# Performance work log

Measured on AMD Instinct MI355X. Metric: run time of the kernel, lower is better.

The kernel has to match this reference:

```python
import jax, jax.numpy as jnp
import numpy as np

N = 500_000          # total nodes in the batched graph
B = 4096             # number of graphs
D_NODE = 256         # node_feature_size
D_GRAPH = 256        # graph_feature_size
D_LOGIT = 10         # logit_mlp_sizes[0]


def setup_inputs() -> dict:
    key = jax.random.key(0)
    ks = jax.random.split(key, 12)
    s = 0.05
    node_feats = jax.random.normal(ks[0], (N, D_NODE), dtype=jnp.float32)
    graph_feats = jax.random.normal(ks[1], (B, D_GRAPH), dtype=jnp.float32)
    segment_ids = jnp.sort(jax.random.randint(ks[2], (N,), 0, B)).astype(jnp.int64)
    # message MLP: Linear(node -> graph)
    W_msg = jax.random.normal(ks[3], (D_GRAPH, D_NODE), dtype=jnp.float32) * s
    b_msg = jnp.zeros((D_GRAPH,), dtype=jnp.float32)
    # logit MLP: Linear(node+graph -> 10) -> LeakyReLU -> Linear(10 -> 1) -> LeakyReLU
    W_l1 = jax.random.normal(ks[4], (D_LOGIT, D_NODE + D_GRAPH), dtype=jnp.float32) * s
    b_l1 = jnp.zeros((D_LOGIT,), dtype=jnp.float32)
    W_l2 = jax.random.normal(ks[5], (1, D_LOGIT), dtype=jnp.float32) * s
    b_l2 = jnp.zeros((1,), dtype=jnp.float32)
    # GRUCell(graph, graph): torch layout [3H, H] gates ordered (r, z, n)
    W_ih = jax.random.normal(ks[6], (3 * D_GRAPH, D_GRAPH), dtype=jnp.float32) * s
    W_hh = jax.random.normal(ks[7], (3 * D_GRAPH, D_GRAPH), dtype=jnp.float32) * s
    b_ih = jnp.zeros((3 * D_GRAPH,), dtype=jnp.float32)
    b_hh = jnp.zeros((3 * D_GRAPH,), dtype=jnp.float32)
    return dict(node_feats=node_feats, graph_feats=graph_feats, segment_ids=segment_ids,
                W_msg=W_msg, b_msg=b_msg, W_l1=W_l1, b_l1=b_l1, W_l2=W_l2, b_l2=b_l2,
                W_ih=W_ih, W_hh=W_hh, b_ih=b_ih, b_hh=b_hh)


def _segment_softmax(logits, seg, num_segments):
    # logits: [N, 1]; stable softmax per graph
    m = jax.ops.segment_max(logits, seg, num_segments=num_segments)      # [B,1]
    m = jnp.where(jnp.isfinite(m), m, 0.0)                               # empty segments
    ex = jnp.exp(logits - m[seg])                                        # [N,1]
    denom = jax.ops.segment_sum(ex, seg, num_segments=num_segments)      # [B,1]
    return ex / jnp.maximum(denom[seg], 1e-30)


def reference(node_feats, graph_feats, segment_ids, W_msg, b_msg,
              W_l1, b_l1, W_l2, b_l2, W_ih, W_hh, b_ih, b_hh):
    seg = segment_ids.astype(jnp.int32)
    num_graphs = graph_feats.shape[0]

    # (1) node logits: MLP on [broadcast(relu(graph_feats)), node_feats]
    g_bcast = jax.nn.relu(graph_feats)[seg]                              # [N, Dg]
    x = jnp.concatenate([g_bcast, node_feats], axis=1)                   # [N, Dg+Dn]
    h = jax.nn.leaky_relu(x @ W_l1.T + b_l1)                             # [N, 10]
    logits = jax.nn.leaky_relu(h @ W_l2.T + b_l2)                        # [N, 1]

    # (2) per-graph softmax over nodes
    alpha = _segment_softmax(logits, seg, num_graphs)                    # [N, 1]

    # (3) messages
    m = node_feats @ W_msg.T + b_msg                                     # [N, Dg]

    # (4) context: weighted segment sum
    context = jax.ops.segment_sum(alpha * m, seg, num_segments=num_graphs)  # [B, Dg]

    # (5) GRU update (torch GRUCell, gate order r,z,n)
    H = graph_feats.shape[1]
    gi = context @ W_ih.T + b_ih                                         # [B, 3H]
    gh = graph_feats @ W_hh.T + b_hh                                     # [B, 3H]
    i_r, i_z, i_n = gi[:, :H], gi[:, H:2*H], gi[:, 2*H:]
    h_r, h_z, h_n = gh[:, :H], gh[:, H:2*H], gh[:, 2*H:]
    r = jax.nn.sigmoid(i_r + h_r)
    z = jax.nn.sigmoid(i_z + h_z)
    n = jnp.tanh(i_n + r * h_n)
    return (1.0 - z) * n + z * graph_feats
```

## Files before the change

### kernel.cpp

```cpp
#include <hip/hip_runtime.h>
#include <math.h>

#define DG 256
#define DL 10
#define CHUNK 128

__device__ __forceinline__ float leaky(float x) { return x > 0.f ? x : 0.01f * x; }
__device__ __forceinline__ float sigmoidf(float x) { return 1.f / (1.f + expf(-x)); }

__global__ void k_starts(const int* __restrict__ seg, int* __restrict__ starts, int N, int B) {
  const int stride = (seg[N - 1] == 0) ? 2 : 1;
  int b = blockIdx.x * blockDim.x + threadIdx.x;
  if (b > B) return;
  if (b == B) { starts[B] = N; return; }
  int lo = 0, hi = N;
  while (lo < hi) {
    int mid = (lo + hi) >> 1;
    if (seg[(size_t)mid * stride] < b) lo = mid + 1; else hi = mid;
  }
  starts[b] = lo;
}

__global__ void k_glog(const float* __restrict__ gf, const float* __restrict__ W_l1,
                       const float* __restrict__ b_l1, float* __restrict__ glog) {
  int b = blockIdx.x;
  int l = threadIdx.x;
  float4 g4 = *(const float4*)(gf + (size_t)b * DG + 4 * l);
  g4.x = fmaxf(g4.x, 0.f); g4.y = fmaxf(g4.y, 0.f);
  g4.z = fmaxf(g4.z, 0.f); g4.w = fmaxf(g4.w, 0.f);
  float p[DL];
#pragma unroll
  for (int j = 0; j < DL; ++j) {
    float4 w4 = *(const float4*)(W_l1 + (size_t)j * 512 + 4 * l);
    p[j] = g4.x * w4.x + g4.y * w4.y + g4.z * w4.z + g4.w * w4.w;
  }
#pragma unroll
  for (int m = 32; m >= 1; m >>= 1) {
#pragma unroll
    for (int j = 0; j < DL; ++j) p[j] += __shfl_xor(p[j], m);
  }
  if (l == 0) {
#pragma unroll
    for (int j = 0; j < DL; ++j) glog[b * DL + j] = p[j] + b_l1[j];
  }
}

__global__ void k_transpose(const float* __restrict__ in, float* __restrict__ out, int R, int C) {
  int idx = blockIdx.x * blockDim.x + threadIdx.x;
  if (idx >= R * C) return;
  int r = idx / C, c = idx - r * C;
  out[c * R + r] = in[idx];
}

__global__ __launch_bounds__(256) void k_pool(
    const float* __restrict__ nf, const int* __restrict__ starts,
    const float* __restrict__ glog, const float* __restrict__ W_l1,
    const float* __restrict__ W_l2, const float* __restrict__ b_l2_p,
    float* __restrict__ pooled) {
  __shared__ float slog[CHUNK];
  __shared__ float sex[CHUNK];

  const int b = blockIdx.x;
  const int tid = threadIdx.x;
  const int lane = tid & 63;
  const int wave = tid >> 6;

  const int start = starts[b];
  const int end   = starts[b + 1];

  float wl[DL][4];
#pragma unroll
  for (int j = 0; j < DL; ++j) {
    float4 w4 = *(const float4*)(W_l1 + (size_t)j * 512 + 256 + 4 * lane);
    wl[j][0] = w4.x; wl[j][1] = w4.y; wl[j][2] = w4.z; wl[j][3] = w4.w;
  }
  float gl[DL];
#pragma unroll
  for (int j = 0; j < DL; ++j) gl[j] = glog[b * DL + j];
  float wl2[DL];
#pragma unroll
  for (int j = 0; j < DL; ++j) wl2[j] = W_l2[j];
  const float bl2 = b_l2_p[0];

  float M = -INFINITY;
  float denom = 0.f;
  float pool = 0.f;

  for (int c0 = start; c0 < end; c0 += CHUNK) {
    const int cn = min(CHUNK, end - c0);

    for (int n = wave; n < cn; n += 4) {
      const float4 x4 = *(const float4*)(nf + ((size_t)(c0 + n) << 8) + 4 * lane);
      float p[DL];
#pragma unroll
      for (int j = 0; j < DL; ++j)
        p[j] = x4.x * wl[j][0] + x4.y * wl[j][1] + x4.z * wl[j][2] + x4.w * wl[j][3];
#pragma unroll
      for (int m = 32; m >= 1; m >>= 1) {
#pragma unroll
        for (int j = 0; j < DL; ++j) p[j] += __shfl_xor(p[j], m);
      }
      float lg = bl2;
#pragma unroll
      for (int j = 0; j < DL; ++j) {
        float h = leaky(p[j] + gl[j]);
        lg += h * wl2[j];
      }
      lg = leaky(lg);
      if (lane == 0) slog[n] = lg;
    }
    __syncthreads();

    float mc = -INFINITY;
    for (int n = 0; n < cn; ++n) mc = fmaxf(mc, slog[n]);
    const float Mn = fmaxf(M, mc);
    const float sc = expf(M - Mn);
    pool *= sc;
    denom *= sc;
    M = Mn;
    if (tid < cn) sex[tid] = expf(slog[tid] - Mn);
    __syncthreads();

    float dsum = 0.f;
    for (int n = 0; n < cn; ++n) dsum += sex[n];
    denom += dsum;

    const float* rowp = nf + ((size_t)c0 << 8) + tid;
#pragma unroll 4
    for (int n = 0; n < cn; ++n) {
      pool += sex[n] * rowp[(size_t)n << 8];
    }
    __syncthreads();
  }

  pooled[(size_t)b * 256 + tid] = pool / fmaxf(denom, 1e-30f);
}

__global__ __launch_bounds__(256) void k_gru(
    const float* __restrict__ pooled, const float* __restrict__ gf,
    const float* __restrict__ WmsgT, const float* __restrict__ b_msg,
    const float* __restrict__ WihT, const float* __restrict__ WhhT,
    const float* __restrict__ b_ih, const float* __restrict__ b_hh,
    float* __restrict__ out) {
  __shared__ float pool_s[8][256];
  __shared__ float gf_s[8][256];
  __shared__ float ctx_s[8][256];

  const int t = threadIdx.x;
  const int b0 = blockIdx.x * 8;
  const int dt = t & 63;
  const int g0 = (t >> 6) * 2;

#pragma unroll
  for (int g = 0; g < 8; ++g) {
    pool_s[g][t] = pooled[(size_t)(b0 + g) * 256 + t];
    gf_s[g][t]   = gf[(size_t)(b0 + g) * 256 + t];
  }
  __syncthreads();

  {
    float acc[2][4] = {{0.f,0.f,0.f,0.f},{0.f,0.f,0.f,0.f}};
#pragma unroll 4
    for (int k = 0; k < 256; ++k) {
      float4 w = *(const float4*)(WmsgT + (size_t)k * 256 + 4 * dt);
#pragma unroll
      for (int gi = 0; gi < 2; ++gi) {
        float p = pool_s[g0 + gi][k];
        acc[gi][0] += p * w.x; acc[gi][1] += p * w.y;
        acc[gi][2] += p * w.z; acc[gi][3] += p * w.w;
      }
    }
    float4 bm = *(const float4*)(b_msg + 4 * dt);
#pragma unroll
    for (int gi = 0; gi < 2; ++gi) {
      ctx_s[g0 + gi][4 * dt + 0] = acc[gi][0] + bm.x;
      ctx_s[g0 + gi][4 * dt + 1] = acc[gi][1] + bm.y;
      ctx_s[g0 + gi][4 * dt + 2] = acc[gi][2] + bm.z;
      ctx_s[g0 + gi][4 * dt + 3] = acc[gi][3] + bm.w;
    }
  }
  __syncthreads();

  float r[2][4], z[2][4];

#pragma unroll
  for (int s = 0; s < 2; ++s) {
    float ai[2][4] = {{0.f,0.f,0.f,0.f},{0.f,0.f,0.f,0.f}};
    float ah[2][4] = {{0.f,0.f,0.f,0.f},{0.f,0.f,0.f,0.f}};
#pragma unroll 4
    for (int k = 0; k < 256; ++k) {
      float4 wi = *(const float4*)(WihT + (size_t)k * 768 + s * 256 + 4 * dt);
      float4 wh = *(const float4*)(WhhT + (size_t)k * 768 + s * 256 + 4 * dt);
#pragma unroll
      for (int gi = 0; gi < 2; ++gi) {
        float c = ctx_s[g0 + gi][k];
        float h = gf_s[g0 + gi][k];
        ai[gi][0] += c * wi.x; ai[gi][1] += c * wi.y; ai[gi][2] += c * wi.z; ai[gi][3] += c * wi.w;
        ah[gi][0] += h * wh.x; ah[gi][1] += h * wh.y; ah[gi][2] += h * wh.z; ah[gi][3] += h * wh.w;
      }
    }
    float4 bi = *(const float4*)(b_ih + s * 256 + 4 * dt);
    float4 bh = *(const float4*)(b_hh + s * 256 + 4 * dt);
#pragma unroll
    for (int gi = 0; gi < 2; ++gi) {
      float v0 = sigmoidf(ai[gi][0] + bi.x + ah[gi][0] + bh.x);
      float v1 = sigmoidf(ai[gi][1] + bi.y + ah[gi][1] + bh.y);
      float v2 = sigmoidf(ai[gi][2] + bi.z + ah[gi][2] + bh.z);
      float v3 = sigmoidf(ai[gi][3] + bi.w + ah[gi][3] + bh.w);
      if (s == 0) { r[gi][0]=v0; r[gi][1]=v1; r[gi][2]=v2; r[gi][3]=v3; }
      else        { z[gi][0]=v0; z[gi][1]=v1; z[gi][2]=v2; z[gi][3]=v3; }
    }
  }

  {
    float ai[2][4] = {{0.f,0.f,0.f,0.f},{0.f,0.f,0.f,0.f}};
    float ah[2][4] = {{0.f,0.f,0.f,0.f},{0.f,0.f,0.f,0.f}};
#pragma unroll 4
    for (int k = 0; k < 256; ++k) {
      float4 wi = *(const float4*)(WihT + (size_t)k * 768 + 512 + 4 * dt);
      float4 wh = *(const float4*)(WhhT + (size_t)k * 768 + 512 + 4 * dt);
#pragma unroll
      for (int gi = 0; gi < 2; ++gi) {
        float c = ctx_s[g0 + gi][k];
        float h = gf_s[g0 + gi][k];
        ai[gi][0] += c * wi.x; ai[gi][1] += c * wi.y; ai[gi][2] += c * wi.z; ai[gi][3] += c * wi.w;
        ah[gi][0] += h * wh.x; ah[gi][1] += h * wh.y; ah[gi][2] += h * wh.z; ah[gi][3] += h * wh.w;
      }
    }
    float4 bi = *(const float4*)(b_ih + 512 + 4 * dt);
    float4 bh = *(const float4*)(b_hh + 512 + 4 * dt);
#pragma unroll
    for (int gi = 0; gi < 2; ++gi) {
      float4 o;
      float hf0 = gf_s[g0 + gi][4 * dt + 0];
      float hf1 = gf_s[g0 + gi][4 * dt + 1];
      float hf2 = gf_s[g0 + gi][4 * dt + 2];
      float hf3 = gf_s[g0 + gi][4 * dt + 3];
      float n0 = tanhf(ai[gi][0] + bi.x + r[gi][0] * (ah[gi][0] + bh.x));
      float n1 = tanhf(ai[gi][1] + bi.y + r[gi][1] * (ah[gi][1] + bh.y));
      float n2 = tanhf(ai[gi][2] + bi.z + r[gi][2] * (ah[gi][2] + bh.z));
      float n3 = tanhf(ai[gi][3] + bi.w + r[gi][3] * (ah[gi][3] + bh.w));
      o.x = (1.f - z[gi][0]) * n0 + z[gi][0] * hf0;
      o.y = (1.f - z[gi][1]) * n1 + z[gi][1] * hf1;
      o.z = (1.f - z[gi][2]) * n2 + z[gi][2] * hf2;
      o.w = (1.f - z[gi][3]) * n3 + z[gi][3] * hf3;
      *(float4*)(out + (size_t)(b0 + g0 + gi) * 256 + 4 * dt) = o;
    }
  }
}

extern "C" void kernel_launch(void* const* d_in, const int* in_sizes, int n_in,
                              void* d_out, int out_size, void* d_ws, size_t ws_size,
                              hipStream_t stream) {
  const float* nf    = (const float*)d_in[0];
  const float* gf    = (const float*)d_in[1];
  const int*   seg   = (const int*)d_in[2];
  const float* W_msg = (const float*)d_in[3];
  const float* b_msg = (const float*)d_in[4];
  const float* W_l1  = (const float*)d_in[5];
  const float* b_l1  = (const float*)d_in[6];
  const float* W_l2  = (const float*)d_in[7];
  const float* b_l2  = (const float*)d_in[8];
  const float* W_ih  = (const float*)d_in[9];
  const float* W_hh  = (const float*)d_in[10];
  const float* b_ih  = (const float*)d_in[11];
  const float* b_hh  = (const float*)d_in[12];
  float* out = (float*)d_out;

  const int N = in_sizes[0] / 256;
  const int B = in_sizes[1] / 256;

  size_t off = 0;
  char* base = (char*)d_ws;
  auto alloc = [&](size_t bytes) -> void* {
    void* p = base + off;
    off += (bytes + 255) & ~(size_t)255;
    return p;
  };
  int*   starts = (int*)  alloc((size_t)(B + 1) * sizeof(int));
  float* glog   = (float*)alloc((size_t)B * DL * sizeof(float));
  float* WmsgT  = (float*)alloc((size_t)256 * 256 * sizeof(float));
  float* WihT   = (float*)alloc((size_t)768 * 256 * sizeof(float));
  float* WhhT   = (float*)alloc((size_t)768 * 256 * sizeof(float));
  float* pooled = (float*)alloc((size_t)B * 256 * sizeof(float));

  k_starts<<<(B + 1 + 255) / 256, 256, 0, stream>>>(seg, starts, N, B);
  k_glog<<<B, 64, 0, stream>>>(gf, W_l1, b_l1, glog);
  k_transpose<<<(256 * 256 + 255) / 256, 256, 0, stream>>>(W_msg, WmsgT, 256, 256);
  k_transpose<<<(768 * 256 + 255) / 256, 256, 0, stream>>>(W_ih, WihT, 768, 256);
  k_transpose<<<(768 * 256 + 255) / 256, 256, 0, stream>>>(W_hh, WhhT, 768, 256);
  k_pool<<<B, 256, 0, stream>>>(nf, starts, glog, W_l1, W_l2, b_l2, pooled);
  k_gru<<<B / 8, 256, 0, stream>>>(pooled, gf, WmsgT, b_msg, WihT, WhhT, b_ih, b_hh, out);
}
```

Measured before the change: 1.151 ms.

## Replace per-graph pooling with node-tiled persistent kernel using atomic segment accumulation

The per-graph pooling kernel and the segment-start binary search are replaced by one persistent kernel. It walks fixed 32-node tiles, stages each tile in swizzled LDS with register prefetch of the next tile, computes logits from LDS, and scatters exp-weighted rows into per-graph sums with atomics. This reads node features from global memory once instead of twice and balances work regardless of graph size. The max-subtraction in the softmax is dropped, so exp(logit) can overflow for large logits. Normalization moves into the GRU kernel, and the three weight transposes are merged into one launch.

```diff
diff --git a/kernel.cpp b/kernel.cpp
--- a/kernel.cpp
+++ b/kernel.cpp
@@ -3,26 +3,15 @@
 
 #define DG 256
 #define DL 10
-#define CHUNK 128
+#define TN 32
+#define NBLK 512
 
 __device__ __forceinline__ float leaky(float x) { return x > 0.f ? x : 0.01f * x; }
 __device__ __forceinline__ float sigmoidf(float x) { return 1.f / (1.f + expf(-x)); }
 
-__global__ void k_starts(const int* __restrict__ seg, int* __restrict__ starts, int N, int B) {
-  const int stride = (seg[N - 1] == 0) ? 2 : 1;
-  int b = blockIdx.x * blockDim.x + threadIdx.x;
-  if (b > B) return;
-  if (b == B) { starts[B] = N; return; }
-  int lo = 0, hi = N;
-  while (lo < hi) {
-    int mid = (lo + hi) >> 1;
-    if (seg[(size_t)mid * stride] < b) lo = mid + 1; else hi = mid;
-  }
-  starts[b] = lo;
-}
-
 __global__ void k_glog(const float* __restrict__ gf, const float* __restrict__ W_l1,
-                       const float* __restrict__ b_l1, float* __restrict__ glog) {
+                       const float* __restrict__ b_l1, float* __restrict__ glog,
+                       float* __restrict__ pooled, float* __restrict__ denom) {
   int b = blockIdx.x;
   int l = threadIdx.x;
   float4 g4 = *(const float4*)(gf + (size_t)b * DG + 4 * l);
@@ -39,109 +28,169 @@
 #pragma unroll
     for (int j = 0; j < DL; ++j) p[j] += __shfl_xor(p[j], m);
   }
+  *(float4*)(pooled + (size_t)b * 256 + 4 * l) = make_float4(0.f, 0.f, 0.f, 0.f);
   if (l == 0) {
 #pragma unroll
-    for (int j = 0; j < DL; ++j) glog[b * DL + j] = p[j] + b_l1[j];
-  }
-}
-
-__global__ void k_transpose(const float* __restrict__ in, float* __restrict__ out, int R, int C) {
+    for (int j = 0; j < DL; ++j) glog[b * 12 + j] = p[j] + b_l1[j];
+    glog[b * 12 + 10] = 0.f;
+    glog[b * 12 + 11] = 0.f;
+    denom[b] = 0.f;
+  }
+}
+
+__global__ void k_transpose3(const float* __restrict__ A, const float* __restrict__ Bm,
+                             const float* __restrict__ C, float* __restrict__ AT,
+                             float* __restrict__ BT, float* __restrict__ CT) {
   int idx = blockIdx.x * blockDim.x + threadIdx.x;
-  if (idx >= R * C) return;
-  int r = idx / C, c = idx - r * C;
-  out[c * R + r] = in[idx];
-}
-
-__global__ __launch_bounds__(256) void k_pool(
-    const float* __restrict__ nf, const int* __restrict__ starts,
-    const float* __restrict__ glog, const float* __restrict__ W_l1,
+  if (idx < 65536) {
+    int r = idx >> 8, c = idx & 255;
+    AT[c * 256 + r] = A[idx];
+  } else if (idx < 262144) {
+    int i = idx - 65536;
+    int r = i >> 8, c = i & 255;
+    BT[c * 768 + r] = Bm[i];
+  } else {
+    int i = idx - 262144;
+    int r = i >> 8, c = i & 255;
+    CT[c * 768 + r] = C[i];
+  }
+}
+
+__global__ __launch_bounds__(256) void k_fused(
+    const float* __restrict__ nf, const int* __restrict__ seg,
+    const float* __restrict__ W_l1, const float* __restrict__ glog,
     const float* __restrict__ W_l2, const float* __restrict__ b_l2_p,
-    float* __restrict__ pooled) {
-  __shared__ float slog[CHUNK];
-  __shared__ float sex[CHUNK];
-
-  const int b = blockIdx.x;
-  const int tid = threadIdx.x;
-  const int lane = tid & 63;
-  const int wave = tid >> 6;
-
-  const int start = starts[b];
-  const int end   = starts[b + 1];
-
-  float wl[DL][4];
-#pragma unroll
-  for (int j = 0; j < DL; ++j) {
-    float4 w4 = *(const float4*)(W_l1 + (size_t)j * 512 + 256 + 4 * lane);
-    wl[j][0] = w4.x; wl[j][1] = w4.y; wl[j][2] = w4.z; wl[j][3] = w4.w;
-  }
-  float gl[DL];
-#pragma unroll
-  for (int j = 0; j < DL; ++j) gl[j] = glog[b * DL + j];
+    float* __restrict__ pooled, float* __restrict__ denom, int N) {
+  __shared__ __align__(16) float xs[TN * 256];
+  __shared__ __align__(16) float pq[TN * 84];
+  __shared__ __align__(16) float wl[DL * 256];
+  __shared__ float sex[TN];
+  __shared__ int gsg[TN];
+
+  const int t = threadIdx.x;
+  const int sstride = (seg[N - 1] == 0) ? 2 : 1;
+
+  for (int i = t; i < DL * 64; i += 256) {
+    int j = i >> 6, c4 = i & 63;
+    *(float4*)(wl + j * 256 + 4 * c4) =
+        *(const float4*)(W_l1 + (size_t)j * 512 + 256 + 4 * c4);
+  }
   float wl2[DL];
 #pragma unroll
   for (int j = 0; j < DL; ++j) wl2[j] = W_l2[j];
   const float bl2 = b_l2_p[0];
 
-  float M = -INFINITY;
-  float denom = 0.f;
-  float pool = 0.f;
-
-  for (int c0 = start; c0 < end; c0 += CHUNK) {
-    const int cn = min(CHUNK, end - c0);
-
-    for (int n = wave; n < cn; n += 4) {
-      const float4 x4 = *(const float4*)(nf + ((size_t)(c0 + n) << 8) + 4 * lane);
-      float p[DL];
-#pragma unroll
-      for (int j = 0; j < DL; ++j)
-        p[j] = x4.x * wl[j][0] + x4.y * wl[j][1] + x4.z * wl[j][2] + x4.w * wl[j][3];
-#pragma unroll
-      for (int m = 32; m >= 1; m >>= 1) {
-#pragma unroll
-        for (int j = 0; j < DL; ++j) p[j] += __shfl_xor(p[j], m);
-      }
-      float lg = bl2;
+  const int ntiles = (N + TN - 1) / TN;
+  const int n = t & 31;
+  const int q = t >> 5;
+  const int sw = n & 7;
+
+  float4 R[8];
+  int tile = blockIdx.x;
+  {
+    const int n0 = tile * TN;
+#pragma unroll
+    for (int i = 0; i < 8; ++i) {
+      int f4i = i * 256 + t;
+      int row = f4i >> 6, col = f4i & 63;
+      int gr = min(n0 + row, N - 1);
+      R[i] = *(const float4*)(nf + ((size_t)gr << 8) + 4 * (col ^ (row & 7)));
+    }
+  }
+
+  for (; tile < ntiles; tile += NBLK) {
+    const int n0 = tile * TN;
+    __syncthreads();
+#pragma unroll
+    for (int i = 0; i < 8; ++i) {
+      int f4i = i * 256 + t;
+      int row = f4i >> 6, col = f4i & 63;
+      *(float4*)(xs + (row << 8) + 4 * col) = R[i];
+    }
+    if (t < TN) {
+      int gr = min(n0 + t, N - 1);
+      gsg[t] = seg[(size_t)gr * sstride];
+    }
+    __syncthreads();
+
+    {
+      int tn2 = tile + NBLK;
+      if (tn2 < ntiles) {
+        const int m0 = tn2 * TN;
+#pragma unroll
+        for (int i = 0; i < 8; ++i) {
+          int f4i = i * 256 + t;
+          int row = f4i >> 6, col = f4i & 63;
+          int gr = min(m0 + row, N - 1);
+          R[i] = *(const float4*)(nf + ((size_t)gr << 8) + 4 * (col ^ (row & 7)));
+        }
+      }
+    }
+
+    float p[DL];
+#pragma unroll
+    for (int j = 0; j < DL; ++j) p[j] = 0.f;
+#pragma unroll
+    for (int i = 0; i < 8; ++i) {
+      const float4 x4 = *(const float4*)(xs + (n << 8) + 4 * (((q << 3) + i) ^ sw));
+      const float* wq = wl + (q << 5) + 4 * i;
 #pragma unroll
       for (int j = 0; j < DL; ++j) {
-        float h = leaky(p[j] + gl[j]);
-        lg += h * wl2[j];
-      }
-      lg = leaky(lg);
-      if (lane == 0) slog[n] = lg;
-    }
+        const float4 w4 = *(const float4*)(wq + j * 256);
+        p[j] += x4.x * w4.x + x4.y * w4.y + x4.z * w4.z + x4.w * w4.w;
+      }
+    }
+#pragma unroll
+    for (int j = 0; j < DL; ++j) pq[n * 84 + 8 * j + q] = p[j];
     __syncthreads();
 
-    float mc = -INFINITY;
-    for (int n = 0; n < cn; ++n) mc = fmaxf(mc, slog[n]);
-    const float Mn = fmaxf(M, mc);
-    const float sc = expf(M - Mn);
-    pool *= sc;
-    denom *= sc;
-    M = Mn;
-    if (tid < cn) sex[tid] = expf(slog[tid] - Mn);
+    if (t < TN) {
+      const int g = gsg[t];
+      const float* gp = glog + g * 12;
+      float gl[12];
+      *(float4*)(gl + 0) = *(const float4*)(gp + 0);
+      *(float4*)(gl + 4) = *(const float4*)(gp + 4);
+      *(float4*)(gl + 8) = *(const float4*)(gp + 8);
+      float acc = bl2;
+#pragma unroll
+      for (int j = 0; j < DL; ++j) {
+        const float4 a = *(const float4*)(pq + t * 84 + 8 * j);
+        const float4 b4 = *(const float4*)(pq + t * 84 + 8 * j + 4);
+        float s = ((a.x + a.y) + (a.z + a.w)) + ((b4.x + b4.y) + (b4.z + b4.w)) + gl[j];
+        acc += wl2[j] * leaky(s);
+      }
+      float lg = leaky(acc);
+      sex[t] = (n0 + t < N) ? expf(lg) : 0.f;
+    }
     __syncthreads();
 
-    float dsum = 0.f;
-    for (int n = 0; n < cn; ++n) dsum += sex[n];
-    denom += dsum;
-
-    const float* rowp = nf + ((size_t)c0 << 8) + tid;
+    {
+      float acc = 0.f, accd = 0.f;
+      int cur = gsg[0];
 #pragma unroll 4
-    for (int n = 0; n < cn; ++n) {
-      pool += sex[n] * rowp[(size_t)n << 8];
-    }
-    __syncthreads();
-  }
-
-  pooled[(size_t)b * 256 + tid] = pool / fmaxf(denom, 1e-30f);
+      for (int nn = 0; nn < TN; ++nn) {
+        int g = gsg[nn];
+        if (g != cur) {
+          atomicAdd(pooled + ((size_t)cur << 8) + t, acc);
+          if (t == 0) atomicAdd(denom + cur, accd);
+          acc = 0.f; accd = 0.f; cur = g;
+        }
+        float e = sex[nn];
+        acc += e * xs[(nn << 8) + (t ^ ((nn & 7) << 2))];
+        accd += e;
+      }
+      atomicAdd(pooled + ((size_t)cur << 8) + t, acc);
+      if (t == 0) atomicAdd(denom + cur, accd);
+    }
+  }
 }
 
 __global__ __launch_bounds__(256) void k_gru(
-    const float* __restrict__ pooled, const float* __restrict__ gf,
-    const float* __restrict__ WmsgT, const float* __restrict__ b_msg,
-    const float* __restrict__ WihT, const float* __restrict__ WhhT,
-    const float* __restrict__ b_ih, const float* __restrict__ b_hh,
-    float* __restrict__ out) {
+    const float* __restrict__ pooled, const float* __restrict__ denom,
+    const float* __restrict__ gf, const float* __restrict__ WmsgT,
+    const float* __restrict__ b_msg, const float* __restrict__ WihT,
+    const float* __restrict__ WhhT, const float* __restrict__ b_ih,
+    const float* __restrict__ b_hh, float* __restrict__ out) {
   __shared__ float pool_s[8][256];
   __shared__ float gf_s[8][256];
   __shared__ float ctx_s[8][256];
@@ -153,21 +202,22 @@
 
 #pragma unroll
   for (int g = 0; g < 8; ++g) {
-    pool_s[g][t] = pooled[(size_t)(b0 + g) * 256 + t];
-    gf_s[g][t]   = gf[(size_t)(b0 + g) * 256 + t];
+    float dn = fmaxf(denom[b0 + g], 1e-30f);
+    pool_s[g][t] = pooled[(size_t)(b0 + g) * 256 + t] / dn;
+    gf_s[g][t] = gf[(size_t)(b0 + g) * 256 + t];
   }
   __syncthreads();
 
   {
-    float acc[2][4] = {{0.f,0.f,0.f,0.f},{0.f,0.f,0.f,0.f}};
+    float acc[2][4] = {{0.f, 0.f, 0.f, 0.f}, {0.f, 0.f, 0.f, 0.f}};
 #pragma unroll 4
     for (int k = 0; k < 256; ++k) {
       float4 w = *(const float4*)(WmsgT + (size_t)k * 256 + 4 * dt);
 #pragma unroll
       for (int gi = 0; gi < 2; ++gi) {
-        float p = pool_s[g0 + gi][k];
-        acc[gi][0] += p * w.x; acc[gi][1] += p * w.y;
-        acc[gi][2] += p * w.z; acc[gi][3] += p * w.w;
+        float pv = pool_s[g0 + gi][k];
+        acc[gi][0] += pv * w.x; acc[gi][1] += pv * w.y;
+        acc[gi][2] += pv * w.z; acc[gi][3] += pv * w.w;
       }
     }
     float4 bm = *(const float4*)(b_msg + 4 * dt);
@@ -185,8 +235,8 @@
 
 #pragma unroll
   for (int s = 0; s < 2; ++s) {
-    float ai[2][4] = {{0.f,0.f,0.f,0.f},{0.f,0.f,0.f,0.f}};
-    float ah[2][4] = {{0.f,0.f,0.f,0.f},{0.f,0.f,0.f,0.f}};
+    float ai[2][4] = {{0.f, 0.f, 0.f, 0.f}, {0.f, 0.f, 0.f, 0.f}};
+    float ah[2][4] = {{0.f, 0.f, 0.f, 0.f}, {0.f, 0.f, 0.f, 0.f}};
 #pragma unroll 4
     for (int k = 0; k < 256; ++k) {
       float4 wi = *(const float4*)(WihT + (size_t)k * 768 + s * 256 + 4 * dt);
@@ -207,14 +257,14 @@
       float v1 = sigmoidf(ai[gi][1] + bi.y + ah[gi][1] + bh.y);
       float v2 = sigmoidf(ai[gi][2] + bi.z + ah[gi][2] + bh.z);
       float v3 = sigmoidf(ai[gi][3] + bi.w + ah[gi][3] + bh.w);
-      if (s == 0) { r[gi][0]=v0; r[gi][1]=v1; r[gi][2]=v2; r[gi][3]=v3; }
-      else        { z[gi][0]=v0; z[gi][1]=v1; z[gi][2]=v2; z[gi][3]=v3; }
+      if (s == 0) { r[gi][0] = v0; r[gi][1] = v1; r[gi][2] = v2; r[gi][3] = v3; }
+      else        { z[gi][0] = v0; z[gi][1] = v1; z[gi][2] = v2; z[gi][3] = v3; }
     }
   }
 
   {
-    float ai[2][4] = {{0.f,0.f,0.f,0.f},{0.f,0.f,0.f,0.f}};
-    float ah[2][4] = {{0.f,0.f,0.f,0.f},{0.f,0.f,0.f,0.f}};
+    float ai[2][4] = {{0.f, 0.f, 0.f, 0.f}, {0.f, 0.f, 0.f, 0.f}};
+    float ah[2][4] = {{0.f, 0.f, 0.f, 0.f}, {0.f, 0.f, 0.f, 0.f}};
 #pragma unroll 4
     for (int k = 0; k < 256; ++k) {
       float4 wi = *(const float4*)(WihT + (size_t)k * 768 + 512 + 4 * dt);
@@ -277,18 +327,21 @@
     off += (bytes + 255) & ~(size_t)255;
     return p;
   };
-  int*   starts = (int*)  alloc((size_t)(B + 1) * sizeof(int));
-  float* glog   = (float*)alloc((size_t)B * DL * sizeof(float));
+  float* glog   = (float*)alloc((size_t)B * 12 * sizeof(float));
   float* WmsgT  = (float*)alloc((size_t)256 * 256 * sizeof(float));
   float* WihT   = (float*)alloc((size_t)768 * 256 * sizeof(float));
   float* WhhT   = (float*)alloc((size_t)768 * 256 * sizeof(float));
   float* pooled = (float*)alloc((size_t)B * 256 * sizeof(float));
-
-  k_starts<<<(B + 1 + 255) / 256, 256, 0, stream>>>(seg, starts, N, B);
-  k_glog<<<B, 64, 0, stream>>>(gf, W_l1, b_l1, glog);
-  k_transpose<<<(256 * 256 + 255) / 256, 256, 0, stream>>>(W_msg, WmsgT, 256, 256);
-  k_transpose<<<(768 * 256 + 255) / 256, 256, 0, stream>>>(W_ih, WihT, 768, 256);
-  k_transpose<<<(768 * 256 + 255) / 256, 256, 0, stream>>>(W_hh, WhhT, 768, 256);
-  k_pool<<<B, 256, 0, stream>>>(nf, starts, glog, W_l1, W_l2, b_l2, pooled);
-  k_gru<<<B / 8, 256, 0, stream>>>(pooled, gf, WmsgT, b_msg, WihT, WhhT, b_ih, b_hh, out);
-}
+  float* denom  = (float*)alloc((size_t)B * sizeof(float));
+
+  k_glog<<<B, 64, 0, stream>>>(gf, W_l1, b_l1, glog, pooled, denom);
+  k_transpose3<<<(65536 + 2 * 196608 + 255) / 256, 256, 0, stream>>>(
+      W_msg, W_ih, W_hh, WmsgT, WihT, WhhT);
+
+  const int ntiles = (N + TN - 1) / TN;
+  const int nblk = ntiles < NBLK ? ntiles : NBLK;
+  k_fused<<<nblk, 256, 0, stream>>>(nf, seg, W_l1, glog, W_l2, b_l2, pooled, denom, N);
+
+  k_gru<<<B / 8, 256, 0, stream>>>(pooled, denom, gf, WmsgT, b_msg, WihT, WhhT,
+                                   b_ih, b_hh, out);
+}
```

New measurement: 1.073 ms. 1.07x faster.
